# Performance work log

Measured on AMD Instinct MI355X. Metric: run time of the kernel, lower is better.

Reference implementation:

```python
import jax, jax.numpy as jnp
import numpy as np
import math

EPS = 1e-5

def _layernorm(x, g, b):
    m = x.mean(-1, keepdims=True)
    v = ((x - m) ** 2).mean(-1, keepdims=True)
    return (x - m) / jnp.sqrt(v + EPS) * g + b

def _skew(emd):
    # RelativePositionalEmbed pad/cat/view skew trick. emd: (B,H,S,S)
    B, H, S, _ = emd.shape
    x = jnp.concatenate([emd, jnp.zeros_like(emd)], -1)   # (B,H,S,2S)
    x = x.reshape(B, H, -1)                                # (B,H,2*S*S)
    l = 2 * S - 1
    extra = (-x.shape[-1]) % l
    x = jnp.concatenate([x, jnp.zeros((B, H, extra), x.dtype)], -1)
    x = x.reshape(B, H, -1, l)
    return x[..., :S, S - 1:]                              # (B,H,S,S)

def setup_inputs() -> dict:
    key = jax.random.key(0)
    ks = jax.random.split(key, 8)
    S, B, D, H, DFF = 1024, 4, 1024, 16, 4096
    dh = D // H
    sc = 1.0 / math.sqrt(D)
    return {
        'x': jax.random.normal(ks[0], (S, B, D), jnp.float32),
        'wq': jax.random.normal(ks[1], (D, D), jnp.float32) * sc,
        'wk': jax.random.normal(ks[2], (D, D), jnp.float32) * sc,
        'wv': jax.random.normal(ks[3], (D, D), jnp.float32) * sc,
        'rel_w': jax.random.normal(ks[4], (B, H, dh, S), jnp.float32) * (1.0 / math.sqrt(dh)),
        'ln1_g': jnp.ones((D,), jnp.float32),
        'ln1_b': jnp.zeros((D,), jnp.float32),
        'ln2_g': jnp.ones((D,), jnp.float32),
        'ln2_b': jnp.zeros((D,), jnp.float32),
        'w1_w': jax.random.normal(ks[5], (DFF, D), jnp.float32) * sc,
        'w1_b': jnp.zeros((DFF,), jnp.float32),
        'w2_w': jax.random.normal(ks[6], (D, DFF), jnp.float32) * (1.0 / math.sqrt(DFF)),
        'w2_b': jnp.zeros((D,), jnp.float32),
    }

def reference(x, wq, wk, wv, rel_w, ln1_g, ln1_b, ln2_g, ln2_b, w1_w, w1_b, w2_w, w2_b):
    S, B, D = x.shape
    H = rel_w.shape[1]
    dh = D // H

    def proj(w):
        y = x @ w.T                      # (S,B,D)
        # torch .view(B,S,H,dh): raw row-major reinterpretation, not a transpose
        return y.reshape(B, S, H, dh).swapaxes(1, 2)  # (B,H,S,dh)

    q, k, v = proj(wq), proj(wk), proj(wv)
    scores = jnp.einsum('bhsd,bhtd->bhst', q * (1.0 / math.sqrt(dh)), k)  # (B,H,S,S)
    # mask=False path: the on-the-fly linear1/linear2 reprojection of qk is
    # computed then discarded in the original; omitted here (dead code).
    emd = jnp.einsum('bhsd,bhdt->bhst', q, rel_w)
    scores = scores + _skew(emd)
    attn = jax.nn.softmax(scores, axis=0)            # softmax over BATCH dim, as in source
    out = jnp.einsum('bhst,bhtd->bhsd', attn, v)     # (B,H,S,dh)
    attn_out = out.reshape(S, B, D)                  # raw reshape, as in source
    h1 = _layernorm(x + attn_out, ln1_g, ln1_b)      # dropout = identity (eval)
    ffn = jnp.maximum(h1 @ w1_w.T + w1_b, 0.0) @ w2_w.T + w2_b
    return _layernorm(h1 + ffn, ln2_g, ln2_b)
```

## Files before the change

### kernel.cpp

```cpp
#include <hip/hip_runtime.h>


typedef unsigned short u16;
typedef unsigned int u32;
typedef __attribute__((ext_vector_type(4))) float f32x4;
typedef __attribute__((ext_vector_type(8))) short bf16x8;
typedef __attribute__((ext_vector_type(4))) u32 u32x4;

__device__ __forceinline__ float bf2f(u16 u) { return __uint_as_float(((u32)u) << 16); }
__device__ __forceinline__ u16 f2bf(float f) {
    u32 u = __float_as_uint(f);
    u += 0x7fffu + ((u >> 16) & 1u);
    return (u16)(u >> 16);
}
template<int DT>
__device__ __forceinline__ float load1(const void* P, size_t idx) {
    return (DT == 0) ? bf2f(((const u16*)P)[idx]) : ((const float*)P)[idx];
}

#define GL16(gp, lp)                                                        \
    __builtin_amdgcn_global_load_lds(                                       \
        (const __attribute__((address_space(1))) void*)(gp),                \
        (__attribute__((address_space(3))) void*)(lp), 16, 0, 0)

__global__ __launch_bounds__(256) void sentinel_ws(float* out, u32 n)
{
    for (u32 i = blockIdx.x * 256 + threadIdx.x; i < n; i += gridDim.x * 256) out[i] = 31000.0f;
}

__global__ __launch_bounds__(256) void cvt_f32_bf16(const float* __restrict__ s,
                                                    u16* __restrict__ d, u32 n)
{
    u32 i = (blockIdx.x * 256 + threadIdx.x) * 4;
    if (i >= n) return;
    float4 v = *(const float4*)(s + i);
    uint2 pk;
    pk.x = (u32)f2bf(v.x) | ((u32)f2bf(v.y) << 16);
    pk.y = (u32)f2bf(v.z) | ((u32)f2bf(v.w) << 16);
    *(uint2*)(d + i) = pk;
}

__global__ __launch_bounds__(256) void relw_tr(const float* __restrict__ relw,
                                               u16* __restrict__ relwT)
{
    __shared__ __align__(16) float T[64][68];
    const int tid = threadIdx.x;
    const int bh = blockIdx.y;
    const int u0 = blockIdx.x << 6;
    {
        const int d = tid >> 2, uq = (tid & 3) << 4;
        const float* rp = relw + (size_t)bh * 65536 + (size_t)d * 1024 + u0 + uq;
#pragma unroll
        for (int i = 0; i < 4; i++)
            *(float4*)&T[d][uq + i * 4] = *(const float4*)(rp + i * 4);
    }
    __syncthreads();
    {
        const int u = tid >> 2, dq = (tid & 3) << 4;
        u32 pk[8];
#pragma unroll
        for (int p = 0; p < 8; p++) {
            float a = T[dq + p * 2][u], b = T[dq + p * 2 + 1][u];
            pk[p] = (u32)f2bf(a) | ((u32)f2bf(b) << 16);
        }
        u16* op = relwT + ((size_t)(bh * 1024 + u0 + u) << 6) + dq;
        *(uint4*)op = *(uint4*)&pk[0];
        *(uint4*)(op + 8) = *(uint4*)&pk[4];
    }
}

__global__ __launch_bounds__(256) void yv_tr(const u16* __restrict__ Yv,
                                             u16* __restrict__ YvT)
{
    __shared__ __align__(16) u16 T[64][72];
    const int tid = threadIdx.x;
    const int bh = blockIdx.y, b = bh >> 4, h = bh & 15;
    const int t0 = blockIdx.x << 6;
    {
        const int r = tid >> 2, cq = (tid & 3) << 4;
        const u16* p = Yv + ((size_t)(b * 1024 + t0 + r) << 10) + h * 64 + cq;
        *(uint4*)&T[r][cq] = *(const uint4*)p;
        *(uint4*)&T[r][cq + 8] = *(const uint4*)(p + 8);
    }
    __syncthreads();
    {
        const int d = tid >> 2, tq = (tid & 3) << 4;
        u16 vals[16];
#pragma unroll
        for (int p = 0; p < 16; p++) vals[p] = T[tq + p][d];
        u16* op = YvT + (((size_t)bh * 64 + d) << 10) + t0 + tq;
        *(uint4*)op = ((uint4*)vals)[0];
        *(uint4*)(op + 8) = ((uint4*)vals)[1];
    }
}

template<int RELU, int OUT_F32, int HAS_BIAS, int SPLIT3, int STAGE,
         int CHX, int CHY>
__global__ __launch_bounds__(256) void mfma_gemm(
    const u16* __restrict__ A, const u16* __restrict__ B,
    const float* __restrict__ bias, void* __restrict__ Cout,
    int M, int N, int K)
{
    __shared__ __align__(16) u16 As[8192];
    __shared__ __align__(16) u16 Bs[8192];
    const int tid = threadIdx.x;
    const int wave = tid >> 6, lane = tid & 63;
    const int quad = lane >> 4, l16 = lane & 15;

    constexpr int S = CHX * CHY;
    const int l = blockIdx.y * gridDim.x + blockIdx.x;
    const int j = l >> 3;
    const int c = (l & 7) + ((j / S) << 3);
    const int w = j % S;
    const int nxc = gridDim.x / CHX;
    const int bx = (c % nxc) * CHX + (w % CHX);
    const int by = (c / nxc) * CHY + (w / CHX);
    const int m0 = by << 7, n0 = bx << 7;
    const int wm = (wave >> 1) << 6, wn = (wave & 1) << 6;

    f32x4 acc[4][4];
#pragma unroll
    for (int i = 0; i < 4; i++)
#pragma unroll
        for (int jj = 0; jj < 4; jj++) acc[i][jj] = (f32x4){0.f, 0.f, 0.f, 0.f};

    if (STAGE) {
        const int srow = tid >> 3;
        const int csw = ((tid & 7) ^ ((tid >> 3) & 7)) << 3;
        const u16* Ags = A + (size_t)(m0 + srow) * K + csw;
        const u16* Bgs = B + (size_t)(n0 + srow) * K + csw;
        const int rx = (l16 & 7) << 3;

        for (int k0 = 0; k0 < K; k0 += 64) {
            __syncthreads();
#pragma unroll
            for (int i = 0; i < 4; i++) {
                GL16(Ags + (size_t)(i * 32) * K + k0, &As[(i * 256 + tid) * 8]);
                GL16(Bgs + (size_t)(i * 32) * K + k0, &Bs[(i * 256 + tid) * 8]);
            }
            __syncthreads();

#pragma unroll
            for (int kk = 0; kk < 2; kk++) {
                bf16x8 af[4], bfr[4];
#pragma unroll
                for (int mi = 0; mi < 4; mi++)
                    af[mi] = *(const bf16x8*)(As + ((wm + mi * 16 + l16) << 6) +
                                              ((((kk * 4 + quad) << 3) ^ rx)));
#pragma unroll
                for (int ni = 0; ni < 4; ni++)
                    bfr[ni] = *(const bf16x8*)(Bs + ((wn + ni * 16 + l16) << 6) +
                                               ((((kk * 4 + quad) << 3) ^ rx)));
#pragma unroll
                for (int mi = 0; mi < 4; mi++)
#pragma unroll
                    for (int ni = 0; ni < 4; ni++)
                        acc[mi][ni] = __builtin_amdgcn_mfma_f32_16x16x32_bf16(
                            af[mi], bfr[ni], acc[mi][ni], 0, 0, 0);
            }
        }
    } else {
        const int r0 = tid >> 2;
        const int csw = ((tid & 3) ^ ((r0 >> 1) & 3)) << 3;
        const u16* Ag0 = A + (size_t)(m0 + r0) * K + csw;
        const u16* Ag1 = A + (size_t)(m0 + r0 + 64) * K + csw;
        const u16* Bg0 = B + (size_t)(n0 + r0) * K + csw;
        const u16* Bg1 = B + (size_t)(n0 + r0 + 64) * K + csw;
        const int pb = ((quad ^ ((l16 >> 1) & 3)) << 3);

        uint4 a0 = *(const uint4*)(Ag0);
        uint4 a1 = *(const uint4*)(Ag1);
        uint4 b0 = *(const uint4*)(Bg0);
        uint4 b1 = *(const uint4*)(Bg1);

        for (int k0 = 0; k0 < K; k0 += 32) {
            __syncthreads();
            *(uint4*)(As + tid * 8)        = a0;
            *(uint4*)(As + 2048 + tid * 8) = a1;
            *(uint4*)(Bs + tid * 8)        = b0;
            *(uint4*)(Bs + 2048 + tid * 8) = b1;
            __syncthreads();

            if (k0 + 32 < K) {
                a0 = *(const uint4*)(Ag0 + k0 + 32);
                a1 = *(const uint4*)(Ag1 + k0 + 32);
                b0 = *(const uint4*)(Bg0 + k0 + 32);
                b1 = *(const uint4*)(Bg1 + k0 + 32);
            }

            bf16x8 af[4], bfr[4];
#pragma unroll
            for (int mi = 0; mi < 4; mi++)
                af[mi] = *(const bf16x8*)(As + ((wm + mi * 16 + l16) << 5) + pb);
#pragma unroll
            for (int ni = 0; ni < 4; ni++)
                bfr[ni] = *(const bf16x8*)(Bs + ((wn + ni * 16 + l16) << 5) + pb);
#pragma unroll
            for (int mi = 0; mi < 4; mi++)
#pragma unroll
                for (int ni = 0; ni < 4; ni++)
                    acc[mi][ni] = __builtin_amdgcn_mfma_f32_16x16x32_bf16(
                        af[mi], bfr[ni], acc[mi][ni], 0, 0, 0);
        }
    }

    float bb[4];
#pragma unroll
    for (int ni = 0; ni < 4; ni++)
        bb[ni] = HAS_BIAS ? bias[n0 + wn + ni * 16 + l16] : 0.f;

#pragma unroll
    for (int mi = 0; mi < 4; mi++) {
#pragma unroll
        for (int ni = 0; ni < 4; ni++) {
            const int col = n0 + wn + ni * 16 + l16;
            const size_t cb = SPLIT3
                ? (((size_t)(col >> 10) << 22) + (size_t)(col & 1023))
                : (size_t)col;
#pragma unroll
            for (int r = 0; r < 4; r++) {
                const int row = m0 + wm + mi * 16 + quad * 4 + r;
                float v = acc[mi][ni][r] + bb[ni];
                if (RELU) v = fmaxf(v, 0.f);
                const size_t idx = SPLIT3 ? (cb + ((size_t)row << 10))
                                          : ((size_t)row * N + cb);
                if (OUT_F32) ((float*)Cout)[idx] = v;
                else ((u16*)Cout)[idx] = f2bf(v);
            }
        }
    }
}

__global__ __launch_bounds__(256) void qk_strip(
    const u16* __restrict__ Yq, const u16* __restrict__ Yk,
    const u16* __restrict__ relwT, u16* __restrict__ scores)
{
    __shared__ __align__(16) u16 lds[26880];
    u16* Ks  = lds;
    u16* Rw  = lds + 4608;
    u16* Eb  = lds + 13824;
    u16* Ssh = lds + 22272;

    const int tid = threadIdx.x;
    const int wave = tid >> 6, lane = tid & 63;
    const int quad = lane >> 4, l16 = lane & 15;
    const int ws = wave >> 1, wt = wave & 1;

    const int linb = blockIdx.y * 16 + blockIdx.x;
    const int swz = (linb & 7) * 128 + (linb >> 3);
    const int si = swz & 15, bh = swz >> 4;
    const int b = bh >> 4, h = bh & 15;
    const int s0 = si << 6;
    const int qb0 = 15 - si;
    const int tau0 = 2 + wt * 2 - ws * 2;

    bf16x8 qf[2][2];
#pragma unroll
    for (int mi = 0; mi < 2; mi++)
#pragma unroll
        for (int kk = 0; kk < 2; kk++)
            qf[mi][kk] = *(const bf16x8*)(Yq +
                ((size_t)(b * 1024 + s0 + ws * 32 + mi * 16 + l16) << 10) +
                h * 64 + kk * 32 + quad * 8);

    const int r = tid >> 2, cq = (tid & 3) << 4;
    const u16* Kg = Yk + ((size_t)(b * 1024 + r) << 10) + h * 64 + cq;
    const u16* Rg = relwT + ((size_t)bh << 16) + cq;

    uint4 kp0, kp1, rp0, rp1, ri0, ri1;
    kp0 = *(const uint4*)(Kg);
    kp1 = *(const uint4*)(Kg + 8);
    {
        const u16* p = Rg + ((size_t)(960 - s0 + r) << 6);
        ri0 = *(const uint4*)p; ri1 = *(const uint4*)(p + 8);
    }
    {
        const int u = 1024 - s0 + r;
        uint4 z = {0, 0, 0, 0};
        rp0 = z; rp1 = z;
        if (u < 1024) {
            const u16* p = Rg + ((size_t)u << 6);
            rp0 = *(const uint4*)p; rp1 = *(const uint4*)(p + 8);
        }
    }

    for (int i = 0; i < 16; i++) {
        const int t0 = i << 6;
        __syncthreads();
        *(uint4*)(Ks + r * 72 + cq)     = kp0;
        *(uint4*)(Ks + r * 72 + cq + 8) = kp1;
        if (i == 0) {
            u16* hb = Rw + (qb0 & 1) * 4608;
            *(uint4*)(hb + r * 72 + cq)     = ri0;
            *(uint4*)(hb + r * 72 + cq + 8) = ri1;
        }
        if (i <= si) {
            u16* hb = Rw + ((qb0 + i + 1) & 1) * 4608;
            *(uint4*)(hb + r * 72 + cq)     = rp0;
            *(uint4*)(hb + r * 72 + cq + 8) = rp1;
        }
        __syncthreads();

        if (i + 1 < 16) {
            const u16* p = Kg + ((size_t)(i + 1) << 16);
            kp0 = *(const uint4*)p; kp1 = *(const uint4*)(p + 8);
        }
        if (i + 1 <= si) {
            const int u = 1024 - s0 + ((i + 1) << 6) + r;
            uint4 z = {0, 0, 0, 0};
            rp0 = z; rp1 = z;
            if (u < 1024) {
                const u16* p = Rg + ((size_t)u << 6);
                rp0 = *(const uint4*)p; rp1 = *(const uint4*)(p + 8);
            }
        }

        f32x4 aqk[2][2];
#pragma unroll
        for (int mi = 0; mi < 2; mi++)
#pragma unroll
            for (int nj = 0; nj < 2; nj++) aqk[mi][nj] = (f32x4){0.f, 0.f, 0.f, 0.f};
#pragma unroll
        for (int kk = 0; kk < 2; kk++)
#pragma unroll
            for (int nj = 0; nj < 2; nj++) {
                bf16x8 kb = *(const bf16x8*)(Ks + (wt * 32 + nj * 16 + l16) * 72 +
                                             kk * 32 + quad * 8);
#pragma unroll
                for (int mi = 0; mi < 2; mi++)
                    aqk[mi][nj] = __builtin_amdgcn_mfma_f32_16x16x32_bf16(
                        qf[mi][kk], kb, aqk[mi][nj], 0, 0, 0);
            }

        const int eact = (i <= si);
        if (eact) {
            const int qb = qb0 + i;
            f32x4 ae[4][2];
#pragma unroll
            for (int uj = 0; uj < 4; uj++)
#pragma unroll
                for (int mi = 0; mi < 2; mi++) ae[uj][mi] = (f32x4){0.f, 0.f, 0.f, 0.f};
#pragma unroll
            for (int kk = 0; kk < 2; kk++)
#pragma unroll
                for (int uj = 0; uj < 4; uj++) {
                    const int tau = tau0 + uj;
                    const u16* hp = Rw + ((qb + (tau >> 2)) & 1) * 4608;
                    bf16x8 ra = *(const bf16x8*)(hp + ((tau & 3) * 16 + l16) * 72 +
                                                 kk * 32 + quad * 8);
#pragma unroll
                    for (int mi = 0; mi < 2; mi++)
                        ae[uj][mi] = __builtin_amdgcn_mfma_f32_16x16x32_bf16(
                            ra, qf[mi][kk], ae[uj][mi], 0, 0, 0);
                }
#pragma unroll
            for (int uj = 0; uj < 4; uj++)
#pragma unroll
                for (int mi = 0; mi < 2; mi++) {
                    const int scol = ws * 32 + mi * 16 + l16;
                    const int cb = (tau0 + uj) * 16 + quad * 4;
                    uint2 pk;
                    pk.x = (u32)f2bf(ae[uj][mi][0]) | ((u32)f2bf(ae[uj][mi][1]) << 16);
                    pk.y = (u32)f2bf(ae[uj][mi][2]) | ((u32)f2bf(ae[uj][mi][3]) << 16);
                    *(uint2*)(Eb + scol * 132 + cb) = pk;
                }
        }

#pragma unroll
        for (int mi = 0; mi < 2; mi++)
#pragma unroll
            for (int nj = 0; nj < 2; nj++)
#pragma unroll
                for (int rr = 0; rr < 4; rr++) {
                    const int sl = ws * 32 + mi * 16 + quad * 4 + rr;
                    const int tl = wt * 32 + nj * 16 + l16;
                    float e = 0.f;
                    if (eact) e = bf2f(Eb[sl * 131 + 63 + tl]);
                    Ssh[sl * 72 + tl] = f2bf(aqk[mi][nj][rr] * 0.125f + e);
                }

        {
            const int row = ws * 32 + (lane >> 1);
            const int col = wt * 32 + ((lane & 1) << 4);
            uint4 v0 = *(const uint4*)(Ssh + row * 72 + col);
            uint4 v1 = *(const uint4*)(Ssh + row * 72 + col + 8);
            u16* op = scores + (((size_t)bh * 1024 + s0 + row) << 10) + t0 + col;
            *(uint4*)op = v0;
            *(uint4*)(op + 8) = v1;
        }
    }
}

__global__ __launch_bounds__(256) void pv_smx(
    const u16* __restrict__ scraw, const u16* __restrict__ YvT,
    float* __restrict__ O)
{
    __shared__ __align__(16) u16 Vt[18432];
    const int tid = threadIdx.x;
    const int w = tid >> 6, lane = tid & 63;
    const int quad = lane >> 4, l16 = lane & 15;

    const int bid = blockIdx.x;
    const int swz = (bid & 7) * 32 + (bid >> 3);
    const int h = swz >> 4, si = swz & 15;
    const int s0 = si << 6;

    const u16* Pl = scraw + ((size_t)(h * 1024 + s0 + w * 16 + l16) << 10) + quad * 8;
    const int sr0 = tid >> 3, sc0 = (tid & 7) << 3;
    const u16* Vg = YvT + ((size_t)h << 16) + ((size_t)sr0 << 10) + sc0;

    f32x4 acc[4][4];
#pragma unroll
    for (int b = 0; b < 4; b++)
#pragma unroll
        for (int j = 0; j < 4; j++) acc[b][j] = (f32x4){0.f, 0.f, 0.f, 0.f};

    u32x4 pc[4][2], pn[4][2], vc[4][2], vn[4][2];
#pragma unroll
    for (int b = 0; b < 4; b++) {
        pc[b][0] = *(const u32x4*)(Pl + ((size_t)b << 24));
        pc[b][1] = *(const u32x4*)(Pl + ((size_t)b << 24) + 32);
        vc[b][0] = *(const u32x4*)(Vg + ((size_t)b << 20));
        vc[b][1] = *(const u32x4*)(Vg + ((size_t)b << 20) + (32 << 10));
    }

    for (int t0 = 0; t0 < 1024; t0 += 64) {
        __syncthreads();
#pragma unroll
        for (int b = 0; b < 4; b++) {
            *(u32x4*)(Vt + b * 4608 + sr0 * 72 + sc0)        = vc[b][0];
            *(u32x4*)(Vt + b * 4608 + (sr0 + 32) * 72 + sc0) = vc[b][1];
        }
        __syncthreads();

        const int more = (t0 + 64 < 1024);
        if (more) {
#pragma unroll
            for (int b = 0; b < 4; b++) {
                pn[b][0] = *(const u32x4*)(Pl + ((size_t)b << 24) + t0 + 64);
                pn[b][1] = *(const u32x4*)(Pl + ((size_t)b << 24) + t0 + 96);
                vn[b][0] = *(const u32x4*)(Vg + ((size_t)b << 20) + t0 + 64);
                vn[b][1] = *(const u32x4*)(Vg + ((size_t)b << 20) + (32 << 10) + t0 + 64);
            }
        }

#pragma unroll
        for (int kk = 0; kk < 2; kk++) {
            u32x4 aw[4];
#pragma unroll
            for (int j = 0; j < 4; j++) {
                float x0[4], x1[4];
#pragma unroll
                for (int b = 0; b < 4; b++) {
                    const u32 wd = pc[b][kk][j];
                    x0[b] = __uint_as_float(wd << 16);
                    x1[b] = __uint_as_float(wd & 0xffff0000u);
                }
                const float m0 = fmaxf(fmaxf(x0[0], x0[1]), fmaxf(x0[2], x0[3]));
                const float m1 = fmaxf(fmaxf(x1[0], x1[1]), fmaxf(x1[2], x1[3]));
                float s0v = 0.f, s1v = 0.f;
#pragma unroll
                for (int b = 0; b < 4; b++) {
                    x0[b] = __expf(x0[b] - m0); s0v += x0[b];
                    x1[b] = __expf(x1[b] - m1); s1v += x1[b];
                }
                const float r0 = 1.f / s0v, r1 = 1.f / s1v;
#pragma unroll
                for (int b = 0; b < 4; b++)
                    aw[b][j] = (u32)f2bf(x0[b] * r0) | ((u32)f2bf(x1[b] * r1) << 16);
            }
#pragma unroll
            for (int b = 0; b < 4; b++) {
                const bf16x8 af = __builtin_bit_cast(bf16x8, aw[b]);
#pragma unroll
                for (int nj = 0; nj < 4; nj++) {
                    bf16x8 bv = *(const bf16x8*)(Vt + b * 4608 + (nj * 16 + l16) * 72 +
                                                 kk * 32 + quad * 8);
                    acc[b][nj] = __builtin_amdgcn_mfma_f32_16x16x32_bf16(
                        af, bv, acc[b][nj], 0, 0, 0);
                }
            }
        }

        if (more) {
#pragma unroll
            for (int b = 0; b < 4; b++) {
                pc[b][0] = pn[b][0]; pc[b][1] = pn[b][1];
                vc[b][0] = vn[b][0]; vc[b][1] = vn[b][1];
            }
        }
    }

#pragma unroll
    for (int b = 0; b < 4; b++)
#pragma unroll
        for (int nj = 0; nj < 4; nj++)
#pragma unroll
            for (int rr = 0; rr < 4; rr++) {
                const int row = s0 + w * 16 + quad * 4 + rr;
                O[((((size_t)(b * 16 + h) << 10) + row) << 6) + nj * 16 + l16] =
                    acc[b][nj][rr];
            }
}

template<int DTA, int OUT_F32>
__global__ __launch_bounds__(256) void add_ln(
    const void* __restrict__ A, const float* __restrict__ Bf,
    const float* __restrict__ g, const float* __restrict__ beta,
    void* __restrict__ out)
{
    const int row = blockIdx.x;
    const int tid = threadIdx.x;
    const size_t base = (size_t)row * 1024;
    float v[4], s1 = 0.f, s2 = 0.f;
#pragma unroll
    for (int k = 0; k < 4; k++) {
        const int c = k * 256 + tid;
        float t = load1<DTA>(A, base + c) + Bf[base + c];
        v[k] = t; s1 += t; s2 += t * t;
    }
#pragma unroll
    for (int m = 1; m < 64; m <<= 1) {
        s1 += __shfl_xor(s1, m, 64);
        s2 += __shfl_xor(s2, m, 64);
    }
    __shared__ float red[8];
    if ((tid & 63) == 0) { red[(tid >> 6) * 2] = s1; red[(tid >> 6) * 2 + 1] = s2; }
    __syncthreads();
    s1 = red[0] + red[2] + red[4] + red[6];
    s2 = red[1] + red[3] + red[5] + red[7];
    const float mean = s1 * (1.f / 1024.f);
    const float var = s2 * (1.f / 1024.f) - mean * mean;
    const float rstd = rsqrtf(var + 1e-5f);
#pragma unroll
    for (int k = 0; k < 4; k++) {
        const int c = k * 256 + tid;
        float o = (v[k] - mean) * rstd * g[c] + beta[c];
        if (OUT_F32) ((float*)out)[base + c] = o;
        else ((u16*)out)[base + c] = f2bf(o);
    }
}

extern "C" void kernel_launch(void* const* d_in, const int* in_sizes, int n_in,
                              void* d_out, int out_size, void* d_ws, size_t ws_size,
                              hipStream_t stream)
{
    const float* x    = (const float*)d_in[0];
    const float* wq   = (const float*)d_in[1];
    const float* wk   = (const float*)d_in[2];
    const float* wv   = (const float*)d_in[3];
    const float* relw = (const float*)d_in[4];
    const float* g1   = (const float*)d_in[5];
    const float* be1  = (const float*)d_in[6];
    const float* g2   = (const float*)d_in[7];
    const float* be2  = (const float*)d_in[8];
    const float* w1   = (const float*)d_in[9];
    const float* b1   = (const float*)d_in[10];
    const float* w2   = (const float*)d_in[11];
    const float* b2   = (const float*)d_in[12];

    const size_t NEEDED = ((size_t)224 << 20);
    if (ws_size < NEEDED) {
        sentinel_ws<<<dim3(1024), dim3(256), 0, stream>>>((float*)d_out, (u32)out_size);
        return;
    }

    char* ws = (char*)d_ws;
    float* O     = (float*)(ws);
    u16*   relwT = (u16*)(ws);
    u16*   Yq    = (u16*)(ws + ((size_t)16 << 20));
    u16*   Yk    = (u16*)(ws + ((size_t)24 << 20));
    u16*   Yv    = (u16*)(ws + ((size_t)32 << 20));
    u16*   h1    = (u16*)(ws + ((size_t)40 << 20));
    u16*   ffn1  = (u16*)(ws + ((size_t)48 << 20));
    float* ffn2  = (float*)(ws + ((size_t)80 << 20));
    u16*   YvT   = (u16*)(ws + ((size_t)80 << 20));
    u16*   sc    = (u16*)(ws + ((size_t)96 << 20));
    u16*   xb    = (u16*)(ws + ((size_t)96 << 20));
    u16*   wqb   = (u16*)(ws + ((size_t)104 << 20));
    u16*   wkb   = (u16*)(ws + ((size_t)106 << 20));
    u16*   wvb   = (u16*)(ws + ((size_t)108 << 20));
    u16*   w1b   = (u16*)(ws + ((size_t)96 << 20));
    u16*   w2b   = (u16*)(ws + ((size_t)104 << 20));

    dim3 blk(256);
    const u32 M4 = 4u << 20, M1 = 1u << 20;

    cvt_f32_bf16<<<dim3(M4 / 1024), blk, 0, stream>>>(x,  xb,  M4);
    cvt_f32_bf16<<<dim3(M1 / 1024), blk, 0, stream>>>(wq, wqb, M1);
    cvt_f32_bf16<<<dim3(M1 / 1024), blk, 0, stream>>>(wk, wkb, M1);
    cvt_f32_bf16<<<dim3(M1 / 1024), blk, 0, stream>>>(wv, wvb, M1);
    relw_tr<<<dim3(16, 64), blk, 0, stream>>>(relw, relwT);

    mfma_gemm<0,0,0,1,1,12,8><<<dim3(24, 32), blk, 0, stream>>>(
        xb, wqb, nullptr, Yq, 4096, 3072, 1024);
    yv_tr<<<dim3(16, 64), blk, 0, stream>>>(Yv, YvT);

    qk_strip<<<dim3(16, 64), blk, 0, stream>>>(Yq, Yk, relwT, sc);
    pv_smx<<<dim3(256), blk, 0, stream>>>(sc, YvT, O);

    add_ln<1,0><<<dim3(4096), blk, 0, stream>>>(x, O, g1, be1, h1);

    cvt_f32_bf16<<<dim3(M4 / 1024), blk, 0, stream>>>(w1, w1b, M4);
    cvt_f32_bf16<<<dim3(M4 / 1024), blk, 0, stream>>>(w2, w2b, M4);

    mfma_gemm<1,0,1,0,1,8,16><<<dim3(32, 32), blk, 0, stream>>>(h1, w1b, b1, ffn1, 4096, 4096, 1024);
    mfma_gemm<0,1,1,0,0,4,8><<<dim3(8, 32), blk, 0, stream>>>(ffn1, w2b, b2, ffn2, 4096, 1024, 4096);

    add_ln<0,1><<<dim3(4096), blk, 0, stream>>>(h1, ffn2, g2, be2, (float*)d_out);
}
```

Baseline: 425.8 us.

## Fuse QK/relative-position score kernel with batch-softmax PV kernel

Merges the score kernel and the softmax-over-batch PV kernel into one attention kernel. Each block now handles all four batches for one (head, 64-row strip), so the bf16 score matrix stays in LDS instead of going through global memory. K and rel_w tiles are loaded with global_load_lds into XOR-swizzled LDS, and the PV phase of the previous tile is overlapped with the loads for the next one. The grid shrinks from 1024 blocks to 256 with a large LDS footprint and one block per CU, so parallelism and latency hiding go down. V is read directly from global memory in the PV phase.

```diff
diff --git a/kernel.cpp b/kernel.cpp
--- a/kernel.cpp
+++ b/kernel.cpp
@@ -231,228 +231,62 @@
     }
 }
 
-__global__ __launch_bounds__(256) void qk_strip(
+__global__ __launch_bounds__(256, 1) void attn_fused(
     const u16* __restrict__ Yq, const u16* __restrict__ Yk,
-    const u16* __restrict__ relwT, u16* __restrict__ scores)
-{
-    __shared__ __align__(16) u16 lds[26880];
+    const u16* __restrict__ relwT, const u16* __restrict__ YvT,
+    float* __restrict__ O)
+{
+    __shared__ __align__(16) u16 lds[76288];
     u16* Ks  = lds;
-    u16* Rw  = lds + 4608;
-    u16* Eb  = lds + 13824;
-    u16* Ssh = lds + 22272;
+    u16* Rw  = lds + 16384;
+    u16* Ssh = lds + 49152;
+    u16* Ebp = lds + 67584;
 
     const int tid = threadIdx.x;
     const int wave = tid >> 6, lane = tid & 63;
     const int quad = lane >> 4, l16 = lane & 15;
     const int ws = wave >> 1, wt = wave & 1;
 
-    const int linb = blockIdx.y * 16 + blockIdx.x;
-    const int swz = (linb & 7) * 128 + (linb >> 3);
-    const int si = swz & 15, bh = swz >> 4;
-    const int b = bh >> 4, h = bh & 15;
-    const int s0 = si << 6;
-    const int qb0 = 15 - si;
-    const int tau0 = 2 + wt * 2 - ws * 2;
-
-    bf16x8 qf[2][2];
-#pragma unroll
-    for (int mi = 0; mi < 2; mi++)
-#pragma unroll
-        for (int kk = 0; kk < 2; kk++)
-            qf[mi][kk] = *(const bf16x8*)(Yq +
-                ((size_t)(b * 1024 + s0 + ws * 32 + mi * 16 + l16) << 10) +
-                h * 64 + kk * 32 + quad * 8);
-
-    const int r = tid >> 2, cq = (tid & 3) << 4;
-    const u16* Kg = Yk + ((size_t)(b * 1024 + r) << 10) + h * 64 + cq;
-    const u16* Rg = relwT + ((size_t)bh << 16) + cq;
-
-    uint4 kp0, kp1, rp0, rp1, ri0, ri1;
-    kp0 = *(const uint4*)(Kg);
-    kp1 = *(const uint4*)(Kg + 8);
-    {
-        const u16* p = Rg + ((size_t)(960 - s0 + r) << 6);
-        ri0 = *(const uint4*)p; ri1 = *(const uint4*)(p + 8);
-    }
-    {
-        const int u = 1024 - s0 + r;
-        uint4 z = {0, 0, 0, 0};
-        rp0 = z; rp1 = z;
-        if (u < 1024) {
-            const u16* p = Rg + ((size_t)u << 6);
-            rp0 = *(const uint4*)p; rp1 = *(const uint4*)(p + 8);
-        }
-    }
-
-    for (int i = 0; i < 16; i++) {
-        const int t0 = i << 6;
-        __syncthreads();
-        *(uint4*)(Ks + r * 72 + cq)     = kp0;
-        *(uint4*)(Ks + r * 72 + cq + 8) = kp1;
-        if (i == 0) {
-            u16* hb = Rw + (qb0 & 1) * 4608;
-            *(uint4*)(hb + r * 72 + cq)     = ri0;
-            *(uint4*)(hb + r * 72 + cq + 8) = ri1;
-        }
-        if (i <= si) {
-            u16* hb = Rw + ((qb0 + i + 1) & 1) * 4608;
-            *(uint4*)(hb + r * 72 + cq)     = rp0;
-            *(uint4*)(hb + r * 72 + cq + 8) = rp1;
-        }
-        __syncthreads();
-
-        if (i + 1 < 16) {
-            const u16* p = Kg + ((size_t)(i + 1) << 16);
-            kp0 = *(const uint4*)p; kp1 = *(const uint4*)(p + 8);
-        }
-        if (i + 1 <= si) {
-            const int u = 1024 - s0 + ((i + 1) << 6) + r;
-            uint4 z = {0, 0, 0, 0};
-            rp0 = z; rp1 = z;
-            if (u < 1024) {
-                const u16* p = Rg + ((size_t)u << 6);
-                rp0 = *(const uint4*)p; rp1 = *(const uint4*)(p + 8);
-            }
-        }
-
-        f32x4 aqk[2][2];
-#pragma unroll
-        for (int mi = 0; mi < 2; mi++)
-#pragma unroll
-            for (int nj = 0; nj < 2; nj++) aqk[mi][nj] = (f32x4){0.f, 0.f, 0.f, 0.f};
-#pragma unroll
-        for (int kk = 0; kk < 2; kk++)
-#pragma unroll
-            for (int nj = 0; nj < 2; nj++) {
-                bf16x8 kb = *(const bf16x8*)(Ks + (wt * 32 + nj * 16 + l16) * 72 +
-                                             kk * 32 + quad * 8);
-#pragma unroll
-                for (int mi = 0; mi < 2; mi++)
-                    aqk[mi][nj] = __builtin_amdgcn_mfma_f32_16x16x32_bf16(
-                        qf[mi][kk], kb, aqk[mi][nj], 0, 0, 0);
-            }
-
-        const int eact = (i <= si);
-        if (eact) {
-            const int qb = qb0 + i;
-            f32x4 ae[4][2];
-#pragma unroll
-            for (int uj = 0; uj < 4; uj++)
-#pragma unroll
-                for (int mi = 0; mi < 2; mi++) ae[uj][mi] = (f32x4){0.f, 0.f, 0.f, 0.f};
-#pragma unroll
-            for (int kk = 0; kk < 2; kk++)
-#pragma unroll
-                for (int uj = 0; uj < 4; uj++) {
-                    const int tau = tau0 + uj;
-                    const u16* hp = Rw + ((qb + (tau >> 2)) & 1) * 4608;
-                    bf16x8 ra = *(const bf16x8*)(hp + ((tau & 3) * 16 + l16) * 72 +
-                                                 kk * 32 + quad * 8);
-#pragma unroll
-                    for (int mi = 0; mi < 2; mi++)
-                        ae[uj][mi] = __builtin_amdgcn_mfma_f32_16x16x32_bf16(
-                            ra, qf[mi][kk], ae[uj][mi], 0, 0, 0);
-                }
-#pragma unroll
-            for (int uj = 0; uj < 4; uj++)
-#pragma unroll
-                for (int mi = 0; mi < 2; mi++) {
-                    const int scol = ws * 32 + mi * 16 + l16;
-                    const int cb = (tau0 + uj) * 16 + quad * 4;
-                    uint2 pk;
-                    pk.x = (u32)f2bf(ae[uj][mi][0]) | ((u32)f2bf(ae[uj][mi][1]) << 16);
-                    pk.y = (u32)f2bf(ae[uj][mi][2]) | ((u32)f2bf(ae[uj][mi][3]) << 16);
-                    *(uint2*)(Eb + scol * 132 + cb) = pk;
-                }
-        }
-
-#pragma unroll
-        for (int mi = 0; mi < 2; mi++)
-#pragma unroll
-            for (int nj = 0; nj < 2; nj++)
-#pragma unroll
-                for (int rr = 0; rr < 4; rr++) {
-                    const int sl = ws * 32 + mi * 16 + quad * 4 + rr;
-                    const int tl = wt * 32 + nj * 16 + l16;
-                    float e = 0.f;
-                    if (eact) e = bf2f(Eb[sl * 131 + 63 + tl]);
-                    Ssh[sl * 72 + tl] = f2bf(aqk[mi][nj][rr] * 0.125f + e);
-                }
-
-        {
-            const int row = ws * 32 + (lane >> 1);
-            const int col = wt * 32 + ((lane & 1) << 4);
-            uint4 v0 = *(const uint4*)(Ssh + row * 72 + col);
-            uint4 v1 = *(const uint4*)(Ssh + row * 72 + col + 8);
-            u16* op = scores + (((size_t)bh * 1024 + s0 + row) << 10) + t0 + col;
-            *(uint4*)op = v0;
-            *(uint4*)(op + 8) = v1;
-        }
-    }
-}
-
-__global__ __launch_bounds__(256) void pv_smx(
-    const u16* __restrict__ scraw, const u16* __restrict__ YvT,
-    float* __restrict__ O)
-{
-    __shared__ __align__(16) u16 Vt[18432];
-    const int tid = threadIdx.x;
-    const int w = tid >> 6, lane = tid & 63;
-    const int quad = lane >> 4, l16 = lane & 15;
-
     const int bid = blockIdx.x;
     const int swz = (bid & 7) * 32 + (bid >> 3);
     const int h = swz >> 4, si = swz & 15;
     const int s0 = si << 6;
-
-    const u16* Pl = scraw + ((size_t)(h * 1024 + s0 + w * 16 + l16) << 10) + quad * 8;
-    const int sr0 = tid >> 3, sc0 = (tid & 7) << 3;
-    const u16* Vg = YvT + ((size_t)h << 16) + ((size_t)sr0 << 10) + sc0;
+    const int qb0 = 15 - si;
+    const int tau0 = 2 + wt * 2 - ws * 2;
+    u16* EbW = Ebp + wave * 2176;
+
+    bf16x8 qf[4][2][2];
+#pragma unroll
+    for (int b = 0; b < 4; b++)
+#pragma unroll
+        for (int mi = 0; mi < 2; mi++)
+#pragma unroll
+            for (int kk = 0; kk < 2; kk++)
+                qf[b][mi][kk] = *(const bf16x8*)(Yq +
+                    ((size_t)(b * 1024 + s0 + ws * 32 + mi * 16 + l16) << 10) +
+                    h * 64 + kk * 32 + quad * 8);
 
     f32x4 acc[4][4];
 #pragma unroll
     for (int b = 0; b < 4; b++)
 #pragma unroll
-        for (int j = 0; j < 4; j++) acc[b][j] = (f32x4){0.f, 0.f, 0.f, 0.f};
-
-    u32x4 pc[4][2], pn[4][2], vc[4][2], vn[4][2];
-#pragma unroll
-    for (int b = 0; b < 4; b++) {
-        pc[b][0] = *(const u32x4*)(Pl + ((size_t)b << 24));
-        pc[b][1] = *(const u32x4*)(Pl + ((size_t)b << 24) + 32);
-        vc[b][0] = *(const u32x4*)(Vg + ((size_t)b << 20));
-        vc[b][1] = *(const u32x4*)(Vg + ((size_t)b << 20) + (32 << 10));
-    }
-
-    for (int t0 = 0; t0 < 1024; t0 += 64) {
-        __syncthreads();
-#pragma unroll
-        for (int b = 0; b < 4; b++) {
-            *(u32x4*)(Vt + b * 4608 + sr0 * 72 + sc0)        = vc[b][0];
-            *(u32x4*)(Vt + b * 4608 + (sr0 + 32) * 72 + sc0) = vc[b][1];
-        }
-        __syncthreads();
-
-        const int more = (t0 + 64 < 1024);
-        if (more) {
-#pragma unroll
-            for (int b = 0; b < 4; b++) {
-                pn[b][0] = *(const u32x4*)(Pl + ((size_t)b << 24) + t0 + 64);
-                pn[b][1] = *(const u32x4*)(Pl + ((size_t)b << 24) + t0 + 96);
-                vn[b][0] = *(const u32x4*)(Vg + ((size_t)b << 20) + t0 + 64);
-                vn[b][1] = *(const u32x4*)(Vg + ((size_t)b << 20) + (32 << 10) + t0 + 64);
-            }
-        }
-
+        for (int nj = 0; nj < 4; nj++) acc[b][nj] = (f32x4){0.f, 0.f, 0.f, 0.f};
+
+    auto phase2 = [&](int t0p) {
 #pragma unroll
         for (int kk = 0; kk < 2; kk++) {
+            u32x4 pcf[4];
+#pragma unroll
+            for (int b = 0; b < 4; b++)
+                pcf[b] = *(const u32x4*)(Ssh + b * 4608 +
+                                         (wave * 16 + l16) * 72 + kk * 32 + quad * 8);
             u32x4 aw[4];
 #pragma unroll
             for (int j = 0; j < 4; j++) {
                 float x0[4], x1[4];
 #pragma unroll
                 for (int b = 0; b < 4; b++) {
-                    const u32 wd = pc[b][kk][j];
+                    const u32 wd = pcf[b][j];
                     x0[b] = __uint_as_float(wd << 16);
                     x1[b] = __uint_as_float(wd & 0xffff0000u);
                 }
@@ -474,22 +308,138 @@
                 const bf16x8 af = __builtin_bit_cast(bf16x8, aw[b]);
 #pragma unroll
                 for (int nj = 0; nj < 4; nj++) {
-                    bf16x8 bv = *(const bf16x8*)(Vt + b * 4608 + (nj * 16 + l16) * 72 +
-                                                 kk * 32 + quad * 8);
+                    bf16x8 bv = *(const bf16x8*)(YvT +
+                        ((size_t)(b * 16 + h) << 16) + ((size_t)(nj * 16 + l16) << 10) +
+                        t0p + kk * 32 + quad * 8);
                     acc[b][nj] = __builtin_amdgcn_mfma_f32_16x16x32_bf16(
                         af, bv, acc[b][nj], 0, 0, 0);
                 }
             }
         }
-
-        if (more) {
-#pragma unroll
-            for (int b = 0; b < 4; b++) {
-                pc[b][0] = pn[b][0]; pc[b][1] = pn[b][1];
-                vc[b][0] = vn[b][0]; vc[b][1] = vn[b][1];
-            }
-        }
-    }
+    };
+
+    for (int i = 0; i < 16; i++) {
+        const int t0 = i << 6;
+
+#pragma unroll
+        for (int k = 0; k < 2; k++) {
+            const int idx = k * 256 + tid;
+            const int row = idx >> 3;
+            const int csw = ((idx & 7) ^ (row & 7)) << 3;
+#pragma unroll
+            for (int b = 0; b < 4; b++)
+                GL16(Yk + ((size_t)(b * 1024 + t0 + row) << 10) + h * 64 + csw,
+                     Ks + b * 4096 + idx * 8);
+        }
+        if (i == 0) {
+#pragma unroll
+            for (int k = 0; k < 2; k++) {
+                const int idx = k * 256 + tid;
+                const int row = idx >> 3;
+                const int csw = ((idx & 7) ^ (row & 7)) << 3;
+#pragma unroll
+                for (int b = 0; b < 4; b++)
+                    GL16(relwT + ((size_t)((b * 16 + h) * 1024 + 960 - s0 + row) << 6) + csw,
+                         Rw + (b * 2 + (qb0 & 1)) * 4096 + idx * 8);
+            }
+        }
+        if (i <= si) {
+            const int sl2 = (qb0 + i + 1) & 1;
+#pragma unroll
+            for (int k = 0; k < 2; k++) {
+                const int idx = k * 256 + tid;
+                const int row = idx >> 3;
+                const int csw = ((idx & 7) ^ (row & 7)) << 3;
+                const int u = 1024 - s0 + t0 + row;
+#pragma unroll
+                for (int b = 0; b < 4; b++) {
+                    u16* dst = Rw + (b * 2 + sl2) * 4096 + idx * 8;
+                    if (u < 1024)
+                        GL16(relwT + ((size_t)((b * 16 + h) * 1024 + u) << 6) + csw, dst);
+                    else
+                        *(u32x4*)dst = (u32x4){0, 0, 0, 0};
+                }
+            }
+        }
+
+        if (i) phase2(t0 - 64);
+        __syncthreads();
+
+        const int eact = (i <= si);
+        const int qb = qb0 + i;
+#pragma unroll
+        for (int b = 0; b < 4; b++) {
+            f32x4 aqk[2][2];
+#pragma unroll
+            for (int mi = 0; mi < 2; mi++)
+#pragma unroll
+                for (int nj = 0; nj < 2; nj++) aqk[mi][nj] = (f32x4){0.f, 0.f, 0.f, 0.f};
+#pragma unroll
+            for (int kk = 0; kk < 2; kk++)
+#pragma unroll
+                for (int nj = 0; nj < 2; nj++) {
+                    const int tr = wt * 32 + nj * 16 + l16;
+                    bf16x8 kb = *(const bf16x8*)(Ks + b * 4096 + tr * 64 +
+                                                 (((kk * 4 + quad) ^ (tr & 7)) << 3));
+#pragma unroll
+                    for (int mi = 0; mi < 2; mi++)
+                        aqk[mi][nj] = __builtin_amdgcn_mfma_f32_16x16x32_bf16(
+                            qf[b][mi][kk], kb, aqk[mi][nj], 0, 0, 0);
+                }
+
+            if (eact) {
+                f32x4 ae[4][2];
+#pragma unroll
+                for (int uj = 0; uj < 4; uj++)
+#pragma unroll
+                    for (int mi = 0; mi < 2; mi++) ae[uj][mi] = (f32x4){0.f, 0.f, 0.f, 0.f};
+#pragma unroll
+                for (int kk = 0; kk < 2; kk++)
+#pragma unroll
+                    for (int uj = 0; uj < 4; uj++) {
+                        const int tau = tau0 + uj;
+                        const int ur = (tau & 3) * 16 + l16;
+                        const u16* hp = Rw + (b * 2 + ((qb + (tau >> 2)) & 1)) * 4096;
+                        bf16x8 ra = *(const bf16x8*)(hp + ur * 64 +
+                                                     (((kk * 4 + quad) ^ (ur & 7)) << 3));
+#pragma unroll
+                        for (int mi = 0; mi < 2; mi++)
+                            ae[uj][mi] = __builtin_amdgcn_mfma_f32_16x16x32_bf16(
+                                ra, qf[b][mi][kk], ae[uj][mi], 0, 0, 0);
+                    }
+#pragma unroll
+                for (int uj = 0; uj < 4; uj++)
+#pragma unroll
+                    for (int mi = 0; mi < 2; mi++) {
+                        const int rloc = mi * 16 + l16;
+                        const int cb = uj * 16 + quad * 4;
+                        uint2 pk;
+                        pk.x = (u32)f2bf(ae[uj][mi][0]) | ((u32)f2bf(ae[uj][mi][1]) << 16);
+                        pk.y = (u32)f2bf(ae[uj][mi][2]) | ((u32)f2bf(ae[uj][mi][3]) << 16);
+                        *(uint2*)(EbW + rloc * 68 + cb) = pk;
+                    }
+            }
+
+#pragma unroll
+            for (int mi = 0; mi < 2; mi++)
+#pragma unroll
+                for (int nj = 0; nj < 2; nj++)
+#pragma unroll
+                    for (int rr = 0; rr < 4; rr++) {
+                        const int slq = mi * 16 + quad * 4 + rr;
+                        const int sl = ws * 32 + slq;
+                        const int tl = wt * 32 + nj * 16 + l16;
+                        float e = 0.f;
+                        if (eact)
+                            e = bf2f(EbW[slq * 68 + 31 + nj * 16 + l16 -
+                                         mi * 16 - quad * 4 - rr]);
+                        Ssh[b * 4608 + sl * 72 + tl] =
+                            f2bf(aqk[mi][nj][rr] * 0.125f + e);
+                    }
+        }
+        __syncthreads();
+    }
+    phase2(960);
 
 #pragma unroll
     for (int b = 0; b < 4; b++)
@@ -497,7 +447,7 @@
         for (int nj = 0; nj < 4; nj++)
 #pragma unroll
             for (int rr = 0; rr < 4; rr++) {
-                const int row = s0 + w * 16 + quad * 4 + rr;
+                const int row = s0 + wave * 16 + quad * 4 + rr;
                 O[((((size_t)(b * 16 + h) << 10) + row) << 6) + nj * 16 + l16] =
                     acc[b][nj][rr];
             }
@@ -567,7 +517,6 @@
 
     char* ws = (char*)d_ws;
     float* O     = (float*)(ws);
-    u16*   relwT = (u16*)(ws);
     u16*   Yq    = (u16*)(ws + ((size_t)16 << 20));
     u16*   Yk    = (u16*)(ws + ((size_t)24 << 20));
     u16*   Yv    = (u16*)(ws + ((size_t)32 << 20));
@@ -575,11 +524,11 @@
     u16*   ffn1  = (u16*)(ws + ((size_t)48 << 20));
     float* ffn2  = (float*)(ws + ((size_t)80 << 20));
     u16*   YvT   = (u16*)(ws + ((size_t)80 << 20));
-    u16*   sc    = (u16*)(ws + ((size_t)96 << 20));
     u16*   xb    = (u16*)(ws + ((size_t)96 << 20));
     u16*   wqb   = (u16*)(ws + ((size_t)104 << 20));
     u16*   wkb   = (u16*)(ws + ((size_t)106 << 20));
     u16*   wvb   = (u16*)(ws + ((size_t)108 << 20));
+    u16*   relwT = (u16*)(ws + ((size_t)112 << 20));
     u16*   w1b   = (u16*)(ws + ((size_t)96 << 20));
     u16*   w2b   = (u16*)(ws + ((size_t)104 << 20));
 
@@ -596,8 +545,7 @@
         xb, wqb, nullptr, Yq, 4096, 3072, 1024);
     yv_tr<<<dim3(16, 64), blk, 0, stream>>>(Yv, YvT);
 
-    qk_strip<<<dim3(16, 64), blk, 0, stream>>>(Yq, Yk, relwT, sc);
-    pv_smx<<<dim3(256), blk, 0, stream>>>(sc, YvT, O);
+    attn_fused<<<dim3(256), blk, 0, stream>>>(Yq, Yk, relwT, YvT, O);
 
     add_ln<1,0><<<dim3(4096), blk, 0, stream>>>(x, O, g1, be1, h1);
 
```

New measurement: 486.1 us. 14.2% more time.
